# Optimization experiments

Measured on AMD Instinct MI355X. Metric: run time of the kernel, lower is better.

## Reference

```python
import jax, jax.numpy as jnp
import numpy as np


def setup_inputs() -> dict:
    key = jax.random.key(0)
    k1, k2 = jax.random.split(key)
    B, S, N, D = 4, 8, 2048, 3
    pred_points = jax.random.normal(k1, (B, S, N, D), dtype=jnp.float32)
    target_points = jax.random.normal(k2, (B, S, N, D), dtype=jnp.float32)
    return {"pred_points": pred_points, "target_points": target_points}


def reference(pred_points, target_points):
    # pred_points, target_points: [B, S, N, 3]
    seq_len = pred_points.shape[1]
    # Pairwise Euclidean distances via the GEMM identity |p-t|^2 = |p|^2 + |t|^2 - 2 p.t
    p2 = jnp.sum(pred_points * pred_points, axis=-1)      # [B,S,N]
    t2 = jnp.sum(target_points * target_points, axis=-1)  # [B,S,M]
    cross = jnp.einsum('bsnd,bsmd->bsnm', pred_points, target_points)  # [B,S,N,M]
    d2 = p2[..., :, None] + t2[..., None, :] - 2.0 * cross
    d = jnp.sqrt(jnp.maximum(d2, 0.0))  # [B,S,N,M]
    # Bidirectional nearest-neighbor min + mean over points
    min_p2t = jnp.min(d, axis=3)  # [B,S,N]
    min_t2p = jnp.min(d, axis=2)  # [B,S,M]
    chamfer = jnp.mean(min_p2t, axis=2) + jnp.mean(min_t2p, axis=2)  # [B,S]
    total_loss = jnp.sum(chamfer, axis=1)  # [B] (sum over timesteps)
    # reduction == 'mean'
    return jnp.mean(total_loss) / seq_len
```

## Files before the change

### kernel.cpp

```cpp
#include <hip/hip_runtime.h>
#include <math.h>

#define N_PTS   2048
#define BLOCK   256
#define NQ      8
#define SLAB    128
#define NSLAB   (N_PTS / SLAB)

__global__ __launch_bounds__(BLOCK) void chamfer_min_kernel(
    const float* __restrict__ pred,
    const float* __restrict__ tgt,
    float* __restrict__ ws)
{
    __shared__ float4 sh[SLAB];

    const int bs   = blockIdx.x;
    const int dir  = blockIdx.y;
    const int slab = blockIdx.z;
    const int tid  = threadIdx.x;

    const float* Abase = (dir ? tgt : pred) + (size_t)bs * N_PTS * 3;
    const float* Bbase = (dir ? pred : tgt) + (size_t)bs * N_PTS * 3;

    if (tid < SLAB) {
        const int j = slab * SLAB + tid;
        const float x = Bbase[3 * j + 0];
        const float y = Bbase[3 * j + 1];
        const float z = Bbase[3 * j + 2];
        sh[tid] = make_float4(x, y, z, x * x + y * y + z * z);
    }
    __syncthreads();

    float nx[NQ], ny[NQ], nz[NQ], p2[NQ], best[NQ];
    #pragma unroll
    for (int k = 0; k < NQ; ++k) {
        const int q = tid + BLOCK * k;
        const float px = Abase[3 * q + 0];
        const float py = Abase[3 * q + 1];
        const float pz = Abase[3 * q + 2];
        nx[k] = -2.0f * px;
        ny[k] = -2.0f * py;
        nz[k] = -2.0f * pz;
        p2[k] = px * px + py * py + pz * pz;
        best[k] = 3.4e38f;
    }

    #pragma unroll 2
    for (int j = 0; j < SLAB; j += 2) {
        const float4 t0 = sh[j];
        const float4 t1 = sh[j + 1];
        #pragma unroll
        for (int k = 0; k < NQ; ++k) {
            const float v0 = fmaf(nx[k], t0.x,
                             fmaf(ny[k], t0.y,
                             fmaf(nz[k], t0.z, t0.w)));
            const float v1 = fmaf(nx[k], t1.x,
                             fmaf(ny[k], t1.y,
                             fmaf(nz[k], t1.z, t1.w)));
            best[k] = fminf(best[k], fminf(v0, v1));
        }
    }

    float* dst = ws + ((size_t)(dir * NSLAB + slab) * 32 + bs) * N_PTS;
    #pragma unroll
    for (int k = 0; k < NQ; ++k)
        dst[tid + BLOCK * k] = p2[k] + best[k];
}

__global__ __launch_bounds__(BLOCK) void chamfer_finalize_kernel(
    const float* __restrict__ ws,
    float* __restrict__ out)
{
    __shared__ float red[BLOCK / 64];
    const int i = blockIdx.x * BLOCK + threadIdx.x;
    const int dir = i >> 16;
    const int bsq = i & 0xFFFF;

    float m = 3.4e38f;
    #pragma unroll
    for (int s = 0; s < NSLAB; ++s) {
        m = fminf(m, ws[(size_t)(dir * NSLAB + s) * 65536 + bsq]);
    }
    float d = sqrtf(fmaxf(m, 0.0f));

    for (int off = 32; off > 0; off >>= 1)
        d += __shfl_down(d, off, 64);
    const int tid = threadIdx.x;
    if ((tid & 63) == 0) red[tid >> 6] = d;
    __syncthreads();
    if (tid == 0) {
        const float blk = red[0] + red[1] + red[2] + red[3];
        atomicAdd(out, blk * (1.0f / 65536.0f));
    }
}

extern "C" void kernel_launch(void* const* d_in, const int* in_sizes, int n_in,
                              void* d_out, int out_size, void* d_ws, size_t ws_size,
                              hipStream_t stream) {
    const float* pred = (const float*)d_in[0];
    const float* tgt  = (const float*)d_in[1];
    float* out = (float*)d_out;
    float* ws = (float*)d_ws;

    hipMemsetAsync(out, 0, sizeof(float), stream);

    dim3 grid(32, 2, NSLAB);
    chamfer_min_kernel<<<grid, BLOCK, 0, stream>>>(pred, tgt, ws);

    chamfer_finalize_kernel<<<131072 / BLOCK, BLOCK, 0, stream>>>(ws, out);
}
```

Measured before the change: 87.06 us.

## Use packed FP32 FMAs with SoA shared layout and more queries per thread

The inner distance loop now uses two-wide float vectors so the compiler can emit packed FP32 FMA instructions, evaluating two target points per instruction. Shared memory moves from an array of float4 to separate x/y/z/w arrays of float pairs to feed those packed operands. The block shrinks to 128 threads, each holding 16 query points, so every thread loads the slab and per-thread register use rises. The finalize kernel is pinned to 256 threads and no longer depends on the main block size.

```diff
diff --git a/kernel.cpp b/kernel.cpp
--- a/kernel.cpp
+++ b/kernel.cpp
@@ -2,17 +2,19 @@
 #include <math.h>
 
 #define N_PTS   2048
-#define BLOCK   256
-#define NQ      8
+#define BLOCK   128
+#define NQ      16
 #define SLAB    128
 #define NSLAB   (N_PTS / SLAB)
+
+typedef float v2f __attribute__((ext_vector_type(2)));
 
 __global__ __launch_bounds__(BLOCK) void chamfer_min_kernel(
     const float* __restrict__ pred,
     const float* __restrict__ tgt,
     float* __restrict__ ws)
 {
-    __shared__ float4 sh[SLAB];
+    __shared__ v2f shx[SLAB / 2], shy[SLAB / 2], shz[SLAB / 2], shw[SLAB / 2];
 
     const int bs   = blockIdx.x;
     const int dir  = blockIdx.y;
@@ -22,42 +24,46 @@
     const float* Abase = (dir ? tgt : pred) + (size_t)bs * N_PTS * 3;
     const float* Bbase = (dir ? pred : tgt) + (size_t)bs * N_PTS * 3;
 
-    if (tid < SLAB) {
+    {
         const int j = slab * SLAB + tid;
         const float x = Bbase[3 * j + 0];
         const float y = Bbase[3 * j + 1];
         const float z = Bbase[3 * j + 2];
-        sh[tid] = make_float4(x, y, z, x * x + y * y + z * z);
+        ((float*)shx)[tid] = x;
+        ((float*)shy)[tid] = y;
+        ((float*)shz)[tid] = z;
+        ((float*)shw)[tid] = x * x + y * y + z * z;
     }
     __syncthreads();
 
-    float nx[NQ], ny[NQ], nz[NQ], p2[NQ], best[NQ];
+    v2f nx2[NQ], ny2[NQ], nz2[NQ];
+    float p2[NQ], best[NQ];
     #pragma unroll
     for (int k = 0; k < NQ; ++k) {
         const int q = tid + BLOCK * k;
         const float px = Abase[3 * q + 0];
         const float py = Abase[3 * q + 1];
         const float pz = Abase[3 * q + 2];
-        nx[k] = -2.0f * px;
-        ny[k] = -2.0f * py;
-        nz[k] = -2.0f * pz;
+        const float ax = -2.0f * px, ay = -2.0f * py, az = -2.0f * pz;
+        nx2[k] = (v2f){ax, ax};
+        ny2[k] = (v2f){ay, ay};
+        nz2[k] = (v2f){az, az};
         p2[k] = px * px + py * py + pz * pz;
         best[k] = 3.4e38f;
     }
 
     #pragma unroll 2
-    for (int j = 0; j < SLAB; j += 2) {
-        const float4 t0 = sh[j];
-        const float4 t1 = sh[j + 1];
+    for (int jj = 0; jj < SLAB / 2; ++jj) {
+        const v2f tx = shx[jj];
+        const v2f ty = shy[jj];
+        const v2f tz = shz[jj];
+        const v2f tw = shw[jj];
         #pragma unroll
         for (int k = 0; k < NQ; ++k) {
-            const float v0 = fmaf(nx[k], t0.x,
-                             fmaf(ny[k], t0.y,
-                             fmaf(nz[k], t0.z, t0.w)));
-            const float v1 = fmaf(nx[k], t1.x,
-                             fmaf(ny[k], t1.y,
-                             fmaf(nz[k], t1.z, t1.w)));
-            best[k] = fminf(best[k], fminf(v0, v1));
+            const v2f v = __builtin_elementwise_fma(nx2[k], tx,
+                          __builtin_elementwise_fma(ny2[k], ty,
+                          __builtin_elementwise_fma(nz2[k], tz, tw)));
+            best[k] = fminf(best[k], fminf(v.x, v.y));
         }
     }
 
@@ -67,20 +73,19 @@
         dst[tid + BLOCK * k] = p2[k] + best[k];
 }
 
-__global__ __launch_bounds__(BLOCK) void chamfer_finalize_kernel(
+__global__ __launch_bounds__(256) void chamfer_finalize_kernel(
     const float* __restrict__ ws,
     float* __restrict__ out)
 {
-    __shared__ float red[BLOCK / 64];
-    const int i = blockIdx.x * BLOCK + threadIdx.x;
+    __shared__ float red[4];
+    const int i = blockIdx.x * 256 + threadIdx.x;
     const int dir = i >> 16;
     const int bsq = i & 0xFFFF;
 
     float m = 3.4e38f;
     #pragma unroll
-    for (int s = 0; s < NSLAB; ++s) {
+    for (int s = 0; s < NSLAB; ++s)
         m = fminf(m, ws[(size_t)(dir * NSLAB + s) * 65536 + bsq]);
-    }
     float d = sqrtf(fmaxf(m, 0.0f));
 
     for (int off = 32; off > 0; off >>= 1)
@@ -107,5 +112,5 @@
     dim3 grid(32, 2, NSLAB);
     chamfer_min_kernel<<<grid, BLOCK, 0, stream>>>(pred, tgt, ws);
 
-    chamfer_finalize_kernel<<<131072 / BLOCK, BLOCK, 0, stream>>>(ws, out);
+    chamfer_finalize_kernel<<<131072 / 256, 256, 0, stream>>>(ws, out);
 }
```

After: 88.08 us. About the same (+1.2%).
